# Performance work log

Hardware: AMD Instinct MI355X
Metric: run time of the kernel (lower is better)

## Reference

```python
import jax, jax.numpy as jnp
import numpy as np

N_BLOCKS = 32
D = 2          # in_out_dim
H = 64         # hidden_dim
LIMIT_RADIUS = 10.0
CLAMP = 1000.0 * LIMIT_RADIUS


def setup_inputs() -> dict:
    key = jax.random.key(0)
    ks = jax.random.split(key, 7)
    N = 131072
    s = 0.1  # small-ish weights so the flow stays well-conditioned
    x = jax.random.normal(ks[0], (N, D), dtype=jnp.float32)
    W1 = jax.random.normal(ks[1], (N_BLOCKS, 1, H), dtype=jnp.float32) * s
    b1 = jax.random.normal(ks[2], (N_BLOCKS, H), dtype=jnp.float32) * s
    W2 = jax.random.normal(ks[3], (N_BLOCKS, H, H), dtype=jnp.float32) * s
    b2 = jax.random.normal(ks[4], (N_BLOCKS, H), dtype=jnp.float32) * s
    W3 = jax.random.normal(ks[5], (N_BLOCKS, H, D), dtype=jnp.float32) * s
    b3 = jax.random.normal(ks[6], (N_BLOCKS, D), dtype=jnp.float32) * s
    loc = jnp.zeros((D,), jnp.float32)        # DiagGaussian trainable loc
    log_scale = jnp.zeros((D,), jnp.float32)  # DiagGaussian trainable log_scale
    return dict(x=x, W1=W1, b1=b1, W2=W2, b2=b2, W3=W3, b3=b3,
                loc=loc, log_scale=log_scale)


def _backward_xz(x, W1, b1, W2, b2, W3, b3):
    """Faithful RealNVP.backward_xz (eval mode: no noise). Flow list is
    [coupling_0, permute_0, ..., coupling_31, permute_31]; inverse pass runs it
    in reverse, applying clamp + move_forward_mask + log_det gating per step."""
    N = x.shape[0]
    z0 = x
    ld0 = jnp.zeros((N,), x.dtype)
    mask0 = jnp.ones((N,), dtype=bool)

    def step(carry, p):
        z, ld_tot, mask = carry
        w1, bb1, w2, bb2, w3, bb3 = p
        # --- Permute('swap').inverse: swap the two halves (D=2 -> column swap), log_det = 0
        z_out = jnp.clip(z[:, ::-1], -CLAMP, CLAMP)
        mask = mask & jnp.all(jnp.abs(z) < LIMIT_RADIUS, axis=1)
        z = jnp.where(mask[:, None], z_out, z)
        # --- AffineCouplingBlock.inverse: split, affine-coupling inverse, merge
        z1, z2 = z[:, :1], z[:, 1:]
        h = jnp.maximum(z1 @ w1 + bb1, 0.0)   # MLP: Linear+ReLU
        h = jnp.maximum(h @ w2 + bb2, 0.0)
        param = h @ w3 + bb3                  # [N, 2] = interleaved (shift, scale)
        shift, scale = param[:, 0::2], param[:, 1::2]
        z2n = (z2 - shift) * jnp.exp(-scale)  # scale_map='exp' inverse
        ld = -jnp.sum(scale, axis=1)
        z_out = jnp.clip(jnp.concatenate([z1, z2n], axis=1), -CLAMP, CLAMP)
        mask = mask & jnp.all(jnp.abs(z) < LIMIT_RADIUS, axis=1)
        z = jnp.where(mask[:, None], z_out, z)
        ld_tot = ld_tot + jnp.where(mask, ld, jnp.zeros_like(ld))
        return (z, ld_tot, mask), None

    rev = lambda a: a[::-1]  # iterate blocks last-to-first
    params = (rev(W1), rev(b1), rev(W2), rev(b2), rev(W3), rev(b3))
    (z, log_det, _), _ = jax.lax.scan(step, (z0, ld0, mask0), params)
    return z, log_det


def reference(x, W1, b1, W2, b2, W3, b3, loc, log_scale):
    # forward_ll(x, noise_amp=0.0, sum=True) in eval mode
    z, log_q = _backward_xz(x, W1, b1, W2, b2, W3, b3)
    log_p0 = (-0.5 * D * jnp.log(2.0 * jnp.pi)
              - jnp.sum(log_scale + 0.5 * ((z - loc) * jnp.exp(-log_scale)) ** 2, axis=1))
    return jnp.sum(log_p0 + log_q)
```

## Files before the change

kernel.cpp:

```cpp
#include <hip/hip_runtime.h>
#include <math.h>

#define NPTS   131072
#define NB     32
#define HD     64
#define KCELL  112
#define PARTS  8
#define PARTN  15
#define LIMIT  10.0f
#define CLAMPV 10000.0f


__global__ __launch_bounds__(256) void build_tab(
    const float* __restrict__ W1, const float* __restrict__ b1,
    const float* __restrict__ W2, const float* __restrict__ b2,
    const float* __restrict__ W3, const float* __restrict__ b3,
    float* __restrict__ ws, float* __restrict__ out)
{
    __shared__ __align__(16) float W2s[HD * HD];
    __shared__ float h1c[16 * HD];
    __shared__ float h2c[16 * 65];
    __shared__ float w1s[HD], b1s[HD], b2s[HD], w3a[HD], w3b[HD];
    __shared__ float sv[17], cv[17];

    const int tid = threadIdx.x;
    const int p = blockIdx.x >> 3;
    const int r = blockIdx.x & 7;
    if (blockIdx.x == 0 && tid == 0) out[0] = 0.0f;

    const int nstart = r * PARTN;
    const int ncell  = min(PARTN, KCELL - nstart);
    const int nn     = ncell + 1;
    const float H    = 20.0f / (float)KCELL;

    for (int i = tid; i < HD * HD; i += 256) W2s[i] = W2[p * HD * HD + i];
    if (tid < HD) {
        w1s[tid] = W1[p * HD + tid];
        b1s[tid] = b1[p * HD + tid];
        b2s[tid] = b2[p * HD + tid];
        w3a[tid] = W3[p * 2 * HD + 2 * tid + 0];
        w3b[tid] = W3[p * 2 * HD + 2 * tid + 1];
    }
    __syncthreads();

    for (int task = tid; task < nn * HD; task += 256) {
        const int n = task >> 6, k = task & 63;
        const float z = fmaf((float)(nstart + n), H, -10.0f);
        h1c[task] = fmaxf(fmaf(w1s[k], z, b1s[k]), 0.0f);
    }
    __syncthreads();

    for (int task = tid; task < nn * HD; task += 256) {
        const int n = task >> 6, j = task & 63;
        float acc = b2s[j];
        const float* h1p = h1c + (n << 6);
        #pragma unroll 8
        for (int k = 0; k < HD; ++k)
            acc = fmaf(W2s[(k << 6) + j], h1p[k], acc);
        h2c[n * 65 + j] = acc;
    }
    __syncthreads();

    const float b30 = b3[p * 2 + 0], b31 = b3[p * 2 + 1];
    if (tid < nn * 2) {
        const int n = tid >> 1, d = tid & 1;
        const float* w3p = d ? w3b : w3a;
        float acc = d ? b31 : b30;
        const float* h2p = h2c + n * 65;
        #pragma unroll 8
        for (int j = 0; j < HD; ++j)
            acc = fmaf(fmaxf(h2p[j], 0.0f), w3p[j], acc);
        (d ? cv : sv)[n] = acc;
    }
    __syncthreads();

    if (tid < ncell) {
        const int c = nstart + tid;
        const float z0 = fmaf((float)c, H, -10.0f);
        const float A = (sv[tid + 1] - sv[tid]) / H;
        const float B = fmaf(-A, z0, sv[tid]);
        const float C = (cv[tid + 1] - cv[tid]) / H;
        const float D = fmaf(-C, z0, cv[tid]);
        ((float4*)ws)[p * KCELL + c] = make_float4(A, B, C, D);
    }
}

__global__ __launch_bounds__(256) void realnvp_eval(
    const float* __restrict__ x,
    const float* __restrict__ ws,
    const float* __restrict__ loc, const float* __restrict__ log_scale,
    float* __restrict__ out)
{
    __shared__ __align__(16) float4 tab[NB * KCELL];

    const int tid = threadIdx.x;
    {
        const uint4* g4 = (const uint4*)ws;
        uint4* l4 = (uint4*)tab;
        #pragma unroll
        for (int i = tid; i < NB * KCELL; i += 256) l4[i] = g4[i];
    }
    __syncthreads();

    const float INVH = (float)KCELL / 20.0f;
    const int g = blockIdx.x * 256 + tid;

    float2 xv = ((const float2*)x)[g];
    float za = xv.x, zb = xv.y;
    float ld = 0.0f;
    bool mask = true;

    for (int t = 0; t < NB; ++t) {
        const int p = NB - 1 - t;

        mask = mask && (fabsf(za) < LIMIT) && (fabsf(zb) < LIMIT);

        const float z1 = mask ? zb : za;
        const float z2 = mask ? za : zb;

        int u = (int)fmaf(z1, INVH, 10.0f * INVH);
        u = min(max(u, 0), KCELL - 1);

        const float4 abcd = tab[p * KCELL + u];
        const float shift = fmaf(abcd.x, z1, abcd.y);
        const float scale = fmaf(abcd.z, z1, abcd.w);
        const float z2n = (z2 - shift) * __expf(-scale);

        if (mask) {
            za = z1;
            zb = fminf(fmaxf(z2n, -CLAMPV), CLAMPV);
            ld -= scale;
        }
    }

    const float l0 = loc[0], l1 = loc[1];
    const float ls0 = log_scale[0], ls1 = log_scale[1];
    const float e0 = __expf(-ls0), e1 = __expf(-ls1);
    const float t0 = (za - l0) * e0, t1 = (zb - l1) * e1;
    float val = -1.8378770664093453f - (ls0 + ls1)
                - 0.5f * (t0 * t0 + t1 * t1) + ld;

    #pragma unroll
    for (int off = 32; off > 0; off >>= 1)
        val += __shfl_down(val, off, 64);
    if ((tid & 63) == 0) atomicAdd(out, val);
}

extern "C" void kernel_launch(void* const* d_in, const int* in_sizes, int n_in,
                              void* d_out, int out_size, void* d_ws, size_t ws_size,
                              hipStream_t stream) {
    const float* x   = (const float*)d_in[0];
    const float* W1  = (const float*)d_in[1];
    const float* b1  = (const float*)d_in[2];
    const float* W2  = (const float*)d_in[3];
    const float* b2  = (const float*)d_in[4];
    const float* W3  = (const float*)d_in[5];
    const float* b3  = (const float*)d_in[6];
    const float* loc = (const float*)d_in[7];
    const float* lsc = (const float*)d_in[8];
    float* out = (float*)d_out;
    float* ws  = (float*)d_ws;

    build_tab<<<NB * PARTS, 256, 0, stream>>>(W1, b1, W2, b2, W3, b3, ws, out);
    realnvp_eval<<<NPTS / 256, 256, 0, stream>>>(x, ws, loc, lsc, out);
}
```

Baseline: 109.1 us.

## Fuse table build and evaluation into one cooperative kernel with grid sync

Merges the table-building kernel and the point-evaluation kernel into a single cooperative launch. Every block first builds a slice of the per-block lookup table, then a grid-wide sync makes the table visible, and the block goes on to evaluate its points. The table build is split into 16 parts of 7 cells instead of 8 parts of 15, so its 512 blocks line up with the evaluation grid and each block does less build work. Build scratch and the table share LDS through a union. Each block now issues one atomic instead of one per wavefront. The cost is relying on all blocks being co-resident and paying for a grid barrier.

```diff
diff --git a/kernel.cpp b/kernel.cpp
--- a/kernel.cpp
+++ b/kernel.cpp
@@ -1,117 +1,125 @@
 #include <hip/hip_runtime.h>
+#include <hip/hip_cooperative_groups.h>
 #include <math.h>
+
+namespace cg = cooperative_groups;
 
 #define NPTS   131072
 #define NB     32
 #define HD     64
 #define KCELL  112
-#define PARTS  8
-#define PARTN  15
+#define PARTS  16
+#define PARTN  7
 #define LIMIT  10.0f
 #define CLAMPV 10000.0f
 
+struct BuildScratch {
+    float W2s[HD * HD];
+    float h1c[8 * HD];
+    float h2c[8 * 65];
+    float w1s[HD], b1s[HD], b2s[HD], w3a[HD], w3b[HD];
+    float sv[9], cv[9];
+};
 
-__global__ __launch_bounds__(256) void build_tab(
+union SharedU {
+    BuildScratch b;
+    float4 tab[NB * KCELL];
+};
+
+__global__ __launch_bounds__(256) void realnvp_fused(
+    const float* __restrict__ x,
     const float* __restrict__ W1, const float* __restrict__ b1,
     const float* __restrict__ W2, const float* __restrict__ b2,
     const float* __restrict__ W3, const float* __restrict__ b3,
+    const float* __restrict__ loc, const float* __restrict__ log_scale,
     float* __restrict__ ws, float* __restrict__ out)
 {
-    __shared__ __align__(16) float W2s[HD * HD];
-    __shared__ float h1c[16 * HD];
-    __shared__ float h2c[16 * 65];
-    __shared__ float w1s[HD], b1s[HD], b2s[HD], w3a[HD], w3b[HD];
-    __shared__ float sv[17], cv[17];
+    __shared__ __align__(16) SharedU sh;
+    __shared__ float red[4];
 
     const int tid = threadIdx.x;
-    const int p = blockIdx.x >> 3;
-    const int r = blockIdx.x & 7;
-    if (blockIdx.x == 0 && tid == 0) out[0] = 0.0f;
+    const int bid = blockIdx.x;
 
+    const int g = bid * 256 + tid;
+    const float2 xv = ((const float2*)x)[g];
+    const float l0 = loc[0], l1 = loc[1];
+    const float ls0 = log_scale[0], ls1 = log_scale[1];
+
+    if (bid == 0 && tid == 0) out[0] = 0.0f;
+
+    const int p = bid >> 4;
+    const int r = bid & 15;
     const int nstart = r * PARTN;
-    const int ncell  = min(PARTN, KCELL - nstart);
-    const int nn     = ncell + 1;
-    const float H    = 20.0f / (float)KCELL;
+    const float Hh = 20.0f / (float)KCELL;
 
-    for (int i = tid; i < HD * HD; i += 256) W2s[i] = W2[p * HD * HD + i];
+    for (int i = tid; i < HD * HD; i += 256) sh.b.W2s[i] = W2[p * HD * HD + i];
     if (tid < HD) {
-        w1s[tid] = W1[p * HD + tid];
-        b1s[tid] = b1[p * HD + tid];
-        b2s[tid] = b2[p * HD + tid];
-        w3a[tid] = W3[p * 2 * HD + 2 * tid + 0];
-        w3b[tid] = W3[p * 2 * HD + 2 * tid + 1];
+        sh.b.w1s[tid] = W1[p * HD + tid];
+        sh.b.b1s[tid] = b1[p * HD + tid];
+        sh.b.b2s[tid] = b2[p * HD + tid];
+        sh.b.w3a[tid] = W3[p * 2 * HD + 2 * tid + 0];
+        sh.b.w3b[tid] = W3[p * 2 * HD + 2 * tid + 1];
     }
     __syncthreads();
 
-    for (int task = tid; task < nn * HD; task += 256) {
+    for (int task = tid; task < 8 * HD; task += 256) {
         const int n = task >> 6, k = task & 63;
-        const float z = fmaf((float)(nstart + n), H, -10.0f);
-        h1c[task] = fmaxf(fmaf(w1s[k], z, b1s[k]), 0.0f);
+        const float z = fmaf((float)(nstart + n), Hh, -10.0f);
+        sh.b.h1c[task] = fmaxf(fmaf(sh.b.w1s[k], z, sh.b.b1s[k]), 0.0f);
     }
     __syncthreads();
 
-    for (int task = tid; task < nn * HD; task += 256) {
+    for (int task = tid; task < 8 * HD; task += 256) {
         const int n = task >> 6, j = task & 63;
-        float acc = b2s[j];
-        const float* h1p = h1c + (n << 6);
+        float acc = sh.b.b2s[j];
+        const float* h1p = sh.b.h1c + (n << 6);
         #pragma unroll 8
         for (int k = 0; k < HD; ++k)
-            acc = fmaf(W2s[(k << 6) + j], h1p[k], acc);
-        h2c[n * 65 + j] = acc;
+            acc = fmaf(sh.b.W2s[(k << 6) + j], h1p[k], acc);
+        sh.b.h2c[n * 65 + j] = acc;
     }
     __syncthreads();
 
     const float b30 = b3[p * 2 + 0], b31 = b3[p * 2 + 1];
-    if (tid < nn * 2) {
+    if (tid < 16) {
         const int n = tid >> 1, d = tid & 1;
-        const float* w3p = d ? w3b : w3a;
+        const float* w3p = d ? sh.b.w3b : sh.b.w3a;
         float acc = d ? b31 : b30;
-        const float* h2p = h2c + n * 65;
+        const float* h2p = sh.b.h2c + n * 65;
         #pragma unroll 8
         for (int j = 0; j < HD; ++j)
             acc = fmaf(fmaxf(h2p[j], 0.0f), w3p[j], acc);
-        (d ? cv : sv)[n] = acc;
+        (d ? sh.b.cv : sh.b.sv)[n] = acc;
     }
     __syncthreads();
 
-    if (tid < ncell) {
+    if (tid < PARTN) {
         const int c = nstart + tid;
-        const float z0 = fmaf((float)c, H, -10.0f);
-        const float A = (sv[tid + 1] - sv[tid]) / H;
-        const float B = fmaf(-A, z0, sv[tid]);
-        const float C = (cv[tid + 1] - cv[tid]) / H;
-        const float D = fmaf(-C, z0, cv[tid]);
-        ((float4*)ws)[p * KCELL + c] = make_float4(A, B, C, D);
+        const float z0 = fmaf((float)c, Hh, -10.0f);
+        const float A = (sh.b.sv[tid + 1] - sh.b.sv[tid]) / Hh;
+        const float B = fmaf(-A, z0, sh.b.sv[tid]);
+        const float C = (sh.b.cv[tid + 1] - sh.b.cv[tid]) / Hh;
+        const float Dd = fmaf(-C, z0, sh.b.cv[tid]);
+        ((float4*)ws)[p * KCELL + c] = make_float4(A, B, C, Dd);
     }
-}
 
-__global__ __launch_bounds__(256) void realnvp_eval(
-    const float* __restrict__ x,
-    const float* __restrict__ ws,
-    const float* __restrict__ loc, const float* __restrict__ log_scale,
-    float* __restrict__ out)
-{
-    __shared__ __align__(16) float4 tab[NB * KCELL];
+    cg::this_grid().sync();
 
-    const int tid = threadIdx.x;
     {
         const uint4* g4 = (const uint4*)ws;
-        uint4* l4 = (uint4*)tab;
+        uint4* l4 = (uint4*)sh.tab;
         #pragma unroll
         for (int i = tid; i < NB * KCELL; i += 256) l4[i] = g4[i];
     }
     __syncthreads();
 
     const float INVH = (float)KCELL / 20.0f;
-    const int g = blockIdx.x * 256 + tid;
-
-    float2 xv = ((const float2*)x)[g];
     float za = xv.x, zb = xv.y;
     float ld = 0.0f;
     bool mask = true;
 
     for (int t = 0; t < NB; ++t) {
-        const int p = NB - 1 - t;
+        const int pp = NB - 1 - t;
 
         mask = mask && (fabsf(za) < LIMIT) && (fabsf(zb) < LIMIT);
 
@@ -121,7 +129,7 @@
         int u = (int)fmaf(z1, INVH, 10.0f * INVH);
         u = min(max(u, 0), KCELL - 1);
 
-        const float4 abcd = tab[p * KCELL + u];
+        const float4 abcd = sh.tab[pp * KCELL + u];
         const float shift = fmaf(abcd.x, z1, abcd.y);
         const float scale = fmaf(abcd.z, z1, abcd.w);
         const float z2n = (z2 - shift) * __expf(-scale);
@@ -133,8 +141,6 @@
         }
     }
 
-    const float l0 = loc[0], l1 = loc[1];
-    const float ls0 = log_scale[0], ls1 = log_scale[1];
     const float e0 = __expf(-ls0), e1 = __expf(-ls1);
     const float t0 = (za - l0) * e0, t1 = (zb - l1) * e1;
     float val = -1.8378770664093453f - (ls0 + ls1)
@@ -143,7 +149,10 @@
     #pragma unroll
     for (int off = 32; off > 0; off >>= 1)
         val += __shfl_down(val, off, 64);
-    if ((tid & 63) == 0) atomicAdd(out, val);
+    if ((tid & 63) == 0) red[tid >> 6] = val;
+    __syncthreads();
+    if (tid == 0)
+        atomicAdd(out, (red[0] + red[1]) + (red[2] + red[3]));
 }
 
 extern "C" void kernel_launch(void* const* d_in, const int* in_sizes, int n_in,
@@ -161,6 +170,12 @@
     float* out = (float*)d_out;
     float* ws  = (float*)d_ws;
 
-    build_tab<<<NB * PARTS, 256, 0, stream>>>(W1, b1, W2, b2, W3, b3, ws, out);
-    realnvp_eval<<<NPTS / 256, 256, 0, stream>>>(x, ws, loc, lsc, out);
+    void* args[] = {
+        (void*)&x, (void*)&W1, (void*)&b1, (void*)&W2, (void*)&b2,
+        (void*)&W3, (void*)&b3, (void*)&loc, (void*)&lsc,
+        (void*)&ws, (void*)&out
+    };
+    hipLaunchCooperativeKernel((void*)realnvp_fused,
+                               dim3(NPTS / 256), dim3(256),
+                               args, 0, stream);
 }
```

Result: slower. 141.3 us (+29.5%).

## Process two points per thread and halve eval grid to amortize table load

Applied to the files above, without the earlier changes.

Each eval thread now handles two points loaded as one float4, so the grid is halved and each block's copy of the full 57KB lookup table into LDS serves twice as many points. The x load is issued before the table copy so its latency overlaps it, and the per-wave atomics are replaced by an LDS reduction with a single atomic per block. In exchange there are fewer blocks (256) to spread across the GPU's compute units. Running two independent dependency chains per thread also adds instruction-level parallelism.

```diff
diff --git a/kernel.cpp b/kernel.cpp
--- a/kernel.cpp
+++ b/kernel.cpp
@@ -92,8 +92,15 @@
     float* __restrict__ out)
 {
     __shared__ __align__(16) float4 tab[NB * KCELL];
+    __shared__ float red[4];
 
     const int tid = threadIdx.x;
+    const int g = blockIdx.x * 256 + tid;
+
+    const float4 xv = ((const float4*)x)[g];
+    const float l0 = loc[0], l1 = loc[1];
+    const float ls0 = log_scale[0], ls1 = log_scale[1];
+
     {
         const uint4* g4 = (const uint4*)ws;
         uint4* l4 = (uint4*)tab;
@@ -103,47 +110,57 @@
     __syncthreads();
 
     const float INVH = (float)KCELL / 20.0f;
-    const int g = blockIdx.x * 256 + tid;
 
-    float2 xv = ((const float2*)x)[g];
-    float za = xv.x, zb = xv.y;
-    float ld = 0.0f;
-    bool mask = true;
+    float za0 = xv.x, zb0 = xv.y;
+    float za1 = xv.z, zb1 = xv.w;
+    float ld0 = 0.0f, ld1 = 0.0f;
+    bool m0 = true, m1 = true;
 
     for (int t = 0; t < NB; ++t) {
         const int p = NB - 1 - t;
+        const float4* tp = tab + p * KCELL;
 
-        mask = mask && (fabsf(za) < LIMIT) && (fabsf(zb) < LIMIT);
+        m0 = m0 && (fabsf(za0) < LIMIT) && (fabsf(zb0) < LIMIT);
+        m1 = m1 && (fabsf(za1) < LIMIT) && (fabsf(zb1) < LIMIT);
 
-        const float z1 = mask ? zb : za;
-        const float z2 = mask ? za : zb;
+        const float z10 = m0 ? zb0 : za0;
+        const float z20 = m0 ? za0 : zb0;
+        const float z11 = m1 ? zb1 : za1;
+        const float z21 = m1 ? za1 : zb1;
 
-        int u = (int)fmaf(z1, INVH, 10.0f * INVH);
-        u = min(max(u, 0), KCELL - 1);
+        int u0 = (int)fmaf(z10, INVH, 10.0f * INVH);
+        int u1 = (int)fmaf(z11, INVH, 10.0f * INVH);
+        u0 = min(max(u0, 0), KCELL - 1);
+        u1 = min(max(u1, 0), KCELL - 1);
 
-        const float4 abcd = tab[p * KCELL + u];
-        const float shift = fmaf(abcd.x, z1, abcd.y);
-        const float scale = fmaf(abcd.z, z1, abcd.w);
-        const float z2n = (z2 - shift) * __expf(-scale);
+        const float4 c0 = tp[u0];
+        const float4 c1 = tp[u1];
 
-        if (mask) {
-            za = z1;
-            zb = fminf(fmaxf(z2n, -CLAMPV), CLAMPV);
-            ld -= scale;
-        }
+        const float sh0 = fmaf(c0.x, z10, c0.y);
+        const float sc0 = fmaf(c0.z, z10, c0.w);
+        const float sh1 = fmaf(c1.x, z11, c1.y);
+        const float sc1 = fmaf(c1.z, z11, c1.w);
+        const float zn0 = (z20 - sh0) * __expf(-sc0);
+        const float zn1 = (z21 - sh1) * __expf(-sc1);
+
+        if (m0) { za0 = z10; zb0 = fminf(fmaxf(zn0, -CLAMPV), CLAMPV); ld0 -= sc0; }
+        if (m1) { za1 = z11; zb1 = fminf(fmaxf(zn1, -CLAMPV), CLAMPV); ld1 -= sc1; }
     }
 
-    const float l0 = loc[0], l1 = loc[1];
-    const float ls0 = log_scale[0], ls1 = log_scale[1];
     const float e0 = __expf(-ls0), e1 = __expf(-ls1);
-    const float t0 = (za - l0) * e0, t1 = (zb - l1) * e1;
-    float val = -1.8378770664093453f - (ls0 + ls1)
-                - 0.5f * (t0 * t0 + t1 * t1) + ld;
+    const float t00 = (za0 - l0) * e0, t01 = (zb0 - l1) * e1;
+    const float t10 = (za1 - l0) * e0, t11 = (zb1 - l1) * e1;
+    float val = 2.0f * (-1.8378770664093453f - (ls0 + ls1))
+                - 0.5f * (t00 * t00 + t01 * t01 + t10 * t10 + t11 * t11)
+                + ld0 + ld1;
 
     #pragma unroll
     for (int off = 32; off > 0; off >>= 1)
         val += __shfl_down(val, off, 64);
-    if ((tid & 63) == 0) atomicAdd(out, val);
+    if ((tid & 63) == 0) red[tid >> 6] = val;
+    __syncthreads();
+    if (tid == 0)
+        atomicAdd(out, (red[0] + red[1]) + (red[2] + red[3]));
 }
 
 extern "C" void kernel_launch(void* const* d_in, const int* in_sizes, int n_in,
@@ -162,5 +179,5 @@
     float* ws  = (float*)d_ws;
 
     build_tab<<<NB * PARTS, 256, 0, stream>>>(W1, b1, W2, b2, W3, b3, ws, out);
-    realnvp_eval<<<NPTS / 256, 256, 0, stream>>>(x, ws, loc, lsc, out);
+    realnvp_eval<<<NPTS / 512, 256, 0, stream>>>(x, ws, loc, lsc, out);
 }
```

Result: faster. 88.01 us (-19.3%).
